# Optimization experiments

Hardware: AMD Instinct MI355X
Metric: run time of the kernel (lower is better)

## Reference

```python
import jax, jax.numpy as jnp
import numpy as np

TEMP = 0.07
EPS = 1e-8
NUM_CLASSES = 7
THRESH = 0.3


def setup_inputs() -> dict:
    key = jax.random.key(0)
    k1, k2, k3, k4, k5 = jax.random.split(key, 5)
    N, H, E, C = 8192, 128, 256, NUM_CLASSES
    reps = jax.random.normal(k1, (N, H), dtype=jnp.float32)
    labels = jax.random.randint(k2, (N,), 0, C, dtype=jnp.int64 if jax.config.jax_enable_x64 else jnp.int32)
    centers = jax.random.normal(k3, (C, E), dtype=jnp.float32)
    fc_w = jax.random.normal(k4, (H, E), dtype=jnp.float32) * (1.0 / np.sqrt(E))
    fc_b = jax.random.normal(k5, (H,), dtype=jnp.float32) * 0.01
    return {"reps": reps, "labels": labels, "centers": centers, "fc_w": fc_w, "fc_b": fc_b}


def reference(reps, labels, centers, fc_w, fc_b):
    # fc(default_centers): [C, H]
    curr_centers = centers @ fc_w.T + fc_b
    pad_labels = jnp.arange(NUM_CLASSES, dtype=labels.dtype)

    all_reps = jnp.concatenate([reps, curr_centers], axis=0)      # [M, H]
    all_labels = jnp.concatenate([labels, pad_labels], axis=0)    # [M]
    B = reps.shape[0]
    M = all_reps.shape[0]

    # cosine similarity via normalized matmul (avoids [B,M,H] broadcast)
    norms = jnp.sqrt(jnp.sum(all_reps * all_reps, axis=-1))
    rn = all_reps / jnp.maximum(norms, 1e-8)[:, None]
    cos = rn[:B] @ rn.T                                           # [B, M]

    scores = (1.0 + cos) * 0.5 + EPS
    eye = (jnp.arange(B)[:, None] == jnp.arange(M)[None, :]).astype(scores.dtype)
    scores = scores * (1.0 - eye) / TEMP
    # torch uses .item() on the max -> a non-differentiable constant
    scores = scores - jax.lax.stop_gradient(jnp.max(scores))
    e = jnp.exp(scores)

    pos_mask = (labels[:, None] == all_labels[None, :]).astype(scores.dtype)  # [B, M]
    mask = 1.0 - eye

    pos_sum = jnp.sum(e * pos_mask * mask, axis=-1)
    neg_sum = jnp.sum(e * (1.0 - pos_mask), axis=-1)
    probs = pos_sum / (pos_sum + neg_sum)
    probs = probs / (jnp.sum(pos_mask * mask, axis=-1) + EPS)

    loss_vec = -jnp.log(probs + EPS)
    loss_mask = (loss_vec > THRESH).astype(loss_vec.dtype)
    denom = jax.lax.stop_gradient(jnp.sum(loss_mask)) + EPS
    loss = jnp.sum(loss_vec * loss_mask) / denom
    return loss
```

## Files before the change

### kernel.cpp

```cpp
#include <hip/hip_runtime.h>
#include <hip/hip_bf16.h>

#define BN 8192
#define MM 8199
#define MP 8208
#define HH 128
#define EE 256
#define GX2 64
#define GY 16
#define NUM_HIST 7

typedef __attribute__((ext_vector_type(8))) short short8;
typedef __attribute__((ext_vector_type(4))) float floatx4;


__global__ __launch_bounds__(256)
void prep_kernel(const float* __restrict__ reps,
                 const int* __restrict__ labels,
                 const float* __restrict__ centers,
                 const float* __restrict__ fc_w,
                 const float* __restrict__ fc_b,
                 __hip_bfloat16* __restrict__ rnt,
                 int* __restrict__ labp,
                 float* __restrict__ tot) {
  const int wid = threadIdx.x >> 6, lane = threadIdx.x & 63;
  const int b = blockIdx.x;
  if (b < 2048) {
    if (threadIdx.x < 8) tot[b * 8 + threadIdx.x] = 0.f;
    const int r = b * 4 + wid;
    float2 v = ((const float2*)(reps + (size_t)r * HH))[lane];
    float ss = v.x * v.x + v.y * v.y;
#pragma unroll
    for (int m = 1; m < 64; m <<= 1) ss += __shfl_xor(ss, m);
    float inv = 1.0f / fmaxf(sqrtf(ss), 1e-8f);
    __hip_bfloat162 h2;
    h2.x = __float2bfloat16(v.x * inv);
    h2.y = __float2bfloat16(v.y * inv);
    size_t o = (size_t)(r >> 4) * 1024 + (lane >> 2) * 64 + (r & 15) * 4 + (lane & 3);
    ((__hip_bfloat162*)rnt)[o] = h2;
    if (lane == 0) labp[r] = labels[r];
  } else {
    __shared__ float currs[7 * HH];
    for (int o = threadIdx.x; o < 7 * HH; o += 256) {
      int c = o >> 7, h = o & 127;
      const float4* ce = (const float4*)(centers + c * EE);
      const float4* w  = (const float4*)(fc_w + h * EE);
      float s = 0.f;
#pragma unroll 4
      for (int j = 0; j < EE / 4; ++j) {
        float4 a = ce[j], bb = w[j];
        s += a.x * bb.x + a.y * bb.y + a.z * bb.z + a.w * bb.w;
      }
      currs[o] = s + fc_b[h];
    }
    __syncthreads();
    for (int k = 0; k < 4; ++k) {
      int c = wid * 4 + k;
      int r = BN + c;
      float2 v = make_float2(0.f, 0.f);
      if (c < 7) v = ((const float2*)(currs + c * HH))[lane];
      float ss = v.x * v.x + v.y * v.y;
#pragma unroll
      for (int m = 1; m < 64; m <<= 1) ss += __shfl_xor(ss, m);
      float inv = 1.0f / fmaxf(sqrtf(ss), 1e-8f);
      __hip_bfloat162 h2;
      h2.x = __float2bfloat16(v.x * inv);
      h2.y = __float2bfloat16(v.y * inv);
      size_t o = (size_t)(r >> 4) * 1024 + (lane >> 2) * 64 + (r & 15) * 4 + (lane & 3);
      ((__hip_bfloat162*)rnt)[o] = h2;
      if (lane == 0) labp[r] = (r < MM) ? r - BN : -1;
    }
  }
}

__global__ __launch_bounds__(256, 2)
void main_kernel(const __hip_bfloat16* __restrict__ rnt,
                 const int* __restrict__ labp,
                 float* __restrict__ tot,
                 float* __restrict__ pos) {
  __shared__ short lbuf[2][2048];
  const int lane = threadIdx.x & 63;
  const int w    = threadIdx.x >> 6;
  const int q = lane >> 4, col = lane & 15;
  const int ibase = blockIdx.x * 128;
  const short* rns = (const short*)rnt;

  short8 afrag[2][4];
  int tix[2];
#pragma unroll
  for (int it = 0; it < 2; ++it) {
    tix[it] = blockIdx.x * 8 + w * 2 + it;
    const short* base = rns + (size_t)tix[it] * 2048 + lane * 8;
    afrag[it][0] = *(const short8*)(base);
    afrag[it][1] = *(const short8*)(base + 512);
    afrag[it][2] = *(const short8*)(base + 1024);
    afrag[it][3] = *(const short8*)(base + 1536);
  }
  int labi[2][4];
#pragma unroll
  for (int it = 0; it < 2; ++it)
#pragma unroll
    for (int r = 0; r < 4; ++r)
      labi[it][r] = labp[ibase + (w * 2 + it) * 16 + q * 4 + r];

  float stot[2][4] = {};
  float spos[2][4] = {};
  const float K2 = 10.30496147f;

  const int t0 = blockIdx.y * 32;
  const int nt = (blockIdx.y == GY - 1) ? 33 : 32;

  *(short8*)&lbuf[0][threadIdx.x * 8] =
      *(const short8*)(rns + (size_t)t0 * 2048 + threadIdx.x * 8);
  __syncthreads();

  for (int s = 0; s < nt; ++s) {
    const int cur = s & 1;
    const int t = t0 + s;
    if (s + 1 < nt)
      *(short8*)&lbuf[cur ^ 1][threadIdx.x * 8] =
          *(const short8*)(rns + (size_t)(t + 1) * 2048 + threadIdx.x * 8);

    const short* lb = &lbuf[cur][0];
    short8 b0 = *(const short8*)(lb + lane * 8);
    short8 b1 = *(const short8*)(lb + 512 + lane * 8);
    short8 b2 = *(const short8*)(lb + 1024 + lane * 8);
    short8 b3 = *(const short8*)(lb + 1536 + lane * 8);
    const int labj = labp[t * 16 + col];

#pragma unroll
    for (int it = 0; it < 2; ++it) {
      floatx4 acc = {0.f, 0.f, 0.f, 0.f};
      acc = __builtin_amdgcn_mfma_f32_16x16x32_bf16(afrag[it][0], b0, acc, 0, 0, 0);
      acc = __builtin_amdgcn_mfma_f32_16x16x32_bf16(afrag[it][1], b1, acc, 0, 0, 0);
      acc = __builtin_amdgcn_mfma_f32_16x16x32_bf16(afrag[it][2], b2, acc, 0, 0, 0);
      acc = __builtin_amdgcn_mfma_f32_16x16x32_bf16(afrag[it][3], b3, acc, 0, 0, 0);
      const bool isdiag = (t == tix[it]);
#pragma unroll
      for (int r = 0; r < 4; ++r) {
        float e = __builtin_amdgcn_exp2f(fmaf(acc[r], K2, -K2));
        if (isdiag && (col == q * 4 + r)) e = 0.f;
        stot[it][r] += e;
        spos[it][r] += (labj == labi[it][r]) ? e : 0.f;
      }
    }
    __syncthreads();
  }

#pragma unroll
  for (int it = 0; it < 2; ++it)
#pragma unroll
    for (int r = 0; r < 4; ++r) {
      float tt = stot[it][r], pp = spos[it][r];
#pragma unroll
      for (int m = 1; m <= 8; m <<= 1) {
        tt += __shfl_xor(tt, m);
        pp += __shfl_xor(pp, m);
      }
      if (col == 0) {
        int i = ibase + (w * 2 + it) * 16 + q * 4 + r;
        atomicAdd(&tot[i], tt);
        atomicAdd(&pos[i], pp);
      }
    }
}

__global__ __launch_bounds__(1024)
void loss_kernel(const float* __restrict__ tot,
                 const float* __restrict__ pos,
                 const int* __restrict__ labels,
                 float* __restrict__ out) {
  __shared__ int hist[NUM_HIST];
  __shared__ float s1[16], s2[16];
  const int tid = threadIdx.x;
  const int lane = tid & 63, wid = tid >> 6;
  if (tid < NUM_HIST) hist[tid] = 0;
  __syncthreads();
  int c0 = 0, c1 = 0, c2 = 0, c3 = 0, c4 = 0, c5 = 0, c6 = 0;
  for (int i = tid; i < BN; i += 1024) {
    int lab = labels[i];
    unsigned long long m0 = __ballot(lab == 0);
    unsigned long long m1 = __ballot(lab == 1);
    unsigned long long m2 = __ballot(lab == 2);
    unsigned long long m3 = __ballot(lab == 3);
    unsigned long long m4 = __ballot(lab == 4);
    unsigned long long m5 = __ballot(lab == 5);
    unsigned long long m6 = __ballot(lab == 6);
    if (lane == 0) {
      c0 += __popcll(m0); c1 += __popcll(m1); c2 += __popcll(m2);
      c3 += __popcll(m3); c4 += __popcll(m4); c5 += __popcll(m5);
      c6 += __popcll(m6);
    }
  }
  if (lane == 0) {
    atomicAdd(&hist[0], c0); atomicAdd(&hist[1], c1); atomicAdd(&hist[2], c2);
    atomicAdd(&hist[3], c3); atomicAdd(&hist[4], c4); atomicAdd(&hist[5], c5);
    atomicAdd(&hist[6], c6);
  }
  __syncthreads();
  const float K2 = 10.30496147f;
  const float epad9 = 9.0f * exp2f(-K2);
  float lsum = 0.f, msum = 0.f;
  for (int i = tid; i < BN; i += 1024) {
    float t = tot[i] - epad9;
    float p = pos[i];
    float c = (float)hist[labels[i]];
    float pr = (p / t) / (c + 1e-8f);
    float lv = -logf(pr + 1e-8f);
    if (lv > 0.3f) { lsum += lv; msum += 1.f; }
  }
#pragma unroll
  for (int m = 1; m < 64; m <<= 1) {
    lsum += __shfl_xor(lsum, m);
    msum += __shfl_xor(msum, m);
  }
  if (lane == 0) { s1[wid] = lsum; s2[wid] = msum; }
  __syncthreads();
  if (wid == 0) {
    float a = (lane < 16) ? s1[lane] : 0.f;
    float b = (lane < 16) ? s2[lane] : 0.f;
#pragma unroll
    for (int m = 1; m < 16; m <<= 1) {
      a += __shfl_xor(a, m);
      b += __shfl_xor(b, m);
    }
    if (lane == 0) out[0] = a / (b + 1e-8f);
  }
}

extern "C" void kernel_launch(void* const* d_in, const int* in_sizes, int n_in,
                              void* d_out, int out_size, void* d_ws, size_t ws_size,
                              hipStream_t stream) {
  const float* reps    = (const float*)d_in[0];
  const int*   labels  = (const int*)d_in[1];
  const float* centers = (const float*)d_in[2];
  const float* fc_w    = (const float*)d_in[3];
  const float* fc_b    = (const float*)d_in[4];
  float* out = (float*)d_out;

  char* ws = (char*)d_ws;
  int* labp   = (int*)(ws + 4096);
  __hip_bfloat16* rnt = (__hip_bfloat16*)(ws + 40960);
  float* tot = (float*)(ws + 40960 + 2101248);
  float* pos = tot + BN;

  prep_kernel<<<2049, 256, 0, stream>>>(reps, labels, centers, fc_w, fc_b, rnt, labp, tot);
  main_kernel<<<dim3(GX2, GY), 256, 0, stream>>>(rnt, labp, tot, pos);
  loss_kernel<<<1, 1024, 0, stream>>>(tot, pos, labels, out);
}
```

Before: 135.4 us.

## Process two column tiles per barrier with register-staged global prefetch

The main loop now handles two 16-column tiles per iteration with a larger double buffer. This halves the number of __syncthreads. The next tiles' global loads go into registers before compute and are written to LDS afterwards, so load latency overlaps the MFMA work. The per-element diagonal masking becomes a rare subtraction on diagonal tiles only, and the odd 33rd tile is handled in a separate tail read straight from global memory. The cost is more registers and twice the LDS, which could reduce occupancy.

```diff
diff --git a/kernel.cpp b/kernel.cpp
--- a/kernel.cpp
+++ b/kernel.cpp
@@ -78,7 +78,7 @@
                  const int* __restrict__ labp,
                  float* __restrict__ tot,
                  float* __restrict__ pos) {
-  __shared__ short lbuf[2][2048];
+  __shared__ short lbuf[2][4096];
   const int lane = threadIdx.x & 63;
   const int w    = threadIdx.x >> 6;
   const int q = lane >> 4, col = lane & 15;
@@ -107,27 +107,7 @@
   float spos[2][4] = {};
   const float K2 = 10.30496147f;
 
-  const int t0 = blockIdx.y * 32;
-  const int nt = (blockIdx.y == GY - 1) ? 33 : 32;
-
-  *(short8*)&lbuf[0][threadIdx.x * 8] =
-      *(const short8*)(rns + (size_t)t0 * 2048 + threadIdx.x * 8);
-  __syncthreads();
-
-  for (int s = 0; s < nt; ++s) {
-    const int cur = s & 1;
-    const int t = t0 + s;
-    if (s + 1 < nt)
-      *(short8*)&lbuf[cur ^ 1][threadIdx.x * 8] =
-          *(const short8*)(rns + (size_t)(t + 1) * 2048 + threadIdx.x * 8);
-
-    const short* lb = &lbuf[cur][0];
-    short8 b0 = *(const short8*)(lb + lane * 8);
-    short8 b1 = *(const short8*)(lb + 512 + lane * 8);
-    short8 b2 = *(const short8*)(lb + 1024 + lane * 8);
-    short8 b3 = *(const short8*)(lb + 1536 + lane * 8);
-    const int labj = labp[t * 16 + col];
-
+  auto accum = [&](short8 b0, short8 b1, short8 b2, short8 b3, int t, int labj) {
 #pragma unroll
     for (int it = 0; it < 2; ++it) {
       floatx4 acc = {0.f, 0.f, 0.f, 0.f};
@@ -135,16 +115,71 @@
       acc = __builtin_amdgcn_mfma_f32_16x16x32_bf16(afrag[it][1], b1, acc, 0, 0, 0);
       acc = __builtin_amdgcn_mfma_f32_16x16x32_bf16(afrag[it][2], b2, acc, 0, 0, 0);
       acc = __builtin_amdgcn_mfma_f32_16x16x32_bf16(afrag[it][3], b3, acc, 0, 0, 0);
-      const bool isdiag = (t == tix[it]);
+      float ev[4];
 #pragma unroll
       for (int r = 0; r < 4; ++r) {
         float e = __builtin_amdgcn_exp2f(fmaf(acc[r], K2, -K2));
-        if (isdiag && (col == q * 4 + r)) e = 0.f;
+        ev[r] = e;
         stot[it][r] += e;
         spos[it][r] += (labj == labi[it][r]) ? e : 0.f;
       }
+      if (t == tix[it]) {
+#pragma unroll
+        for (int r = 0; r < 4; ++r)
+          if (col == q * 4 + r) { stot[it][r] -= ev[r]; spos[it][r] -= ev[r]; }
+      }
+    }
+  };
+
+  const int t0 = blockIdx.y * 32;
+
+  {
+    const short* g = rns + (size_t)t0 * 2048 + threadIdx.x * 8;
+    *(short8*)&lbuf[0][threadIdx.x * 8] = *(const short8*)g;
+    *(short8*)&lbuf[0][2048 + threadIdx.x * 8] = *(const short8*)(g + 2048);
+  }
+  __syncthreads();
+
+  for (int p = 0; p < 16; ++p) {
+    const int cur = p & 1;
+    const int t = t0 + p * 2;
+    short8 nv0, nv1;
+    const bool more = (p < 15);
+    if (more) {
+      const short* g = rns + (size_t)(t + 2) * 2048 + threadIdx.x * 8;
+      nv0 = *(const short8*)g;
+      nv1 = *(const short8*)(g + 2048);
+    }
+    const int labj0 = labp[t * 16 + col];
+    const int labj1 = labp[t * 16 + 16 + col];
+
+    const short* lb = &lbuf[cur][0];
+    short8 b0 = *(const short8*)(lb + lane * 8);
+    short8 b1 = *(const short8*)(lb + 512 + lane * 8);
+    short8 b2 = *(const short8*)(lb + 1024 + lane * 8);
+    short8 b3 = *(const short8*)(lb + 1536 + lane * 8);
+    short8 c0 = *(const short8*)(lb + 2048 + lane * 8);
+    short8 c1 = *(const short8*)(lb + 2560 + lane * 8);
+    short8 c2 = *(const short8*)(lb + 3072 + lane * 8);
+    short8 c3 = *(const short8*)(lb + 3584 + lane * 8);
+
+    accum(b0, b1, b2, b3, t, labj0);
+    accum(c0, c1, c2, c3, t + 1, labj1);
+
+    if (more) {
+      *(short8*)&lbuf[cur ^ 1][threadIdx.x * 8] = nv0;
+      *(short8*)&lbuf[cur ^ 1][2048 + threadIdx.x * 8] = nv1;
     }
     __syncthreads();
+  }
+
+  if (blockIdx.y == GY - 1) {
+    const short* g = rns + (size_t)512 * 2048 + lane * 8;
+    short8 b0 = *(const short8*)(g);
+    short8 b1 = *(const short8*)(g + 512);
+    short8 b2 = *(const short8*)(g + 1024);
+    short8 b3 = *(const short8*)(g + 1536);
+    accum(b0, b1, b2, b3, 512, labp[512 * 16 + col]);
   }
 
 #pragma unroll
```

Result: faster. 131.1 us (-3.2%).
